# Optimization experiments

Measured on AMD Instinct MI355X. Metric: run time of the kernel, lower is better.

Reference implementation:

```python
import jax, jax.numpy as jnp
import numpy as np

B, T, F, H = 2048, 129, 128, 128  # batch, window, features, hidden


def setup_inputs() -> dict:
    key = jax.random.key(0)
    ks = jax.random.split(key, 7)
    s = 0.05
    return {
        "x": jax.random.normal(ks[0], (B, T - 1, F), jnp.float32),
        "w_lin": jax.random.normal(ks[1], (1, 2 * H + T - 1), jnp.float32) * s,  # attn Linear weight
        "b_lin": jax.random.normal(ks[2], (1,), jnp.float32) * s,
        "w_ih": jax.random.normal(ks[3], (4 * H, F), jnp.float32) * s,  # LSTM input weights (i,f,g,o)
        "w_hh": jax.random.normal(ks[4], (4 * H, H), jnp.float32) * s,
        "b_ih": jax.random.normal(ks[5], (4 * H,), jnp.float32) * s,
        "b_hh": jax.random.normal(ks[6], (4 * H,), jnp.float32) * s,
    }


def _forward(x, w_lin, b_lin, w_ih, w_hh, b_ih, b_hh):
    # x: [B, T-1, F]
    nb, tm1, nf = x.shape
    nh = w_hh.shape[1]
    # Split attention linear weight into the parts applied to h, c, and x-row.
    wh, wc, wx = w_lin[0, :nh], w_lin[0, nh:2 * nh], w_lin[0, 2 * nh:]
    # x.permute(0,2,1) part of the concat is time-invariant: precompute its score.
    s_x = jnp.einsum('btf,t->bf', x, wx)  # [B, F]
    bias = b_ih + b_hh

    def step(carry, xt):
        h, c = carry  # [B, H] each
        # score for feature k = wh.h + wc.c + wx.x[:,k,:] + b  (h/c terms equal for all k)
        scores = (h @ wh + c @ wc + b_lin[0])[:, None] + s_x  # [B, F]
        a = jax.nn.softmax(scores, axis=1)
        xa = a * xt  # attended input at time t, [B, F]
        gates = xa @ w_ih.T + h @ w_hh.T + bias  # [B, 4H]
        i, f, g, o = jnp.split(gates, 4, axis=1)  # torch LSTM gate order
        c_new = jax.nn.sigmoid(f) * c + jax.nn.sigmoid(i) * jnp.tanh(g)
        h_new = jax.nn.sigmoid(o) * jnp.tanh(c_new)
        return (h_new, c_new), (xa, h_new)

    h0 = jnp.zeros((nb, nh), x.dtype)
    _, (xa_seq, h_seq) = jax.lax.scan(step, (h0, h0), x.transpose(1, 0, 2))
    x_atn = xa_seq.transpose(1, 0, 2)  # [B, T-1, F]
    x_enc = h_seq.transpose(1, 0, 2)   # [B, T-1, H]
    return x_atn, x_enc


def reference(x, w_lin, b_lin, w_ih, w_hh, b_ih, b_hh):
    return _forward(x, w_lin, b_lin, w_ih, w_hh, b_ih, b_hh)
```

## Files before the change

### kernel.cpp

```cpp
#include <hip/hip_runtime.h>
#include <hip/hip_bf16.h>

typedef __attribute__((ext_vector_type(8))) short bf16x8;
typedef __attribute__((ext_vector_type(4))) float f32x4;

#define NB 2048
#define TT 128
#define FF 128
#define HH 128
#define NG 512

__device__ __forceinline__ unsigned short f2bf(float x) {
  union { float f; unsigned u; } v; v.f = x;
  unsigned r = (v.u + 0x7fffu + ((v.u >> 16) & 1u)) >> 16;
  return (unsigned short)r;
}
__device__ __forceinline__ unsigned cvtpk_bf16(float lo, float hi) {
  unsigned r;
  asm("v_cvt_pk_bf16_f32 %0, %1, %2" : "=v"(r) : "v"(lo), "v"(hi));
  return r;
}
__device__ __forceinline__ float frcp(float x) { return __builtin_amdgcn_rcpf(x); }
__device__ __forceinline__ float sigf(float x) { return frcp(1.f + __expf(-x)); }
__device__ __forceinline__ float tanh_(float x) {
  float e = __expf(-2.f * x);
  return (1.f - e) * frcp(1.f + e);
}
__device__ __forceinline__ unsigned swzb(int row, int kbyte) {
  return (unsigned)(row * 256 + (kbyte ^ ((row & 7) << 4)));
}
__device__ __forceinline__ void barrier_lds() {
  asm volatile("s_waitcnt lgkmcnt(0)\n\ts_barrier" ::: "memory");
}

__global__ void k_prep(const float* __restrict__ w_ih, const float* __restrict__ w_hh,
                       const float* __restrict__ b_ih, const float* __restrict__ b_hh,
                       unsigned short* __restrict__ wihb, unsigned short* __restrict__ whhb,
                       float* __restrict__ bias) {
  int g = blockIdx.x * blockDim.x + threadIdx.x;
  int gs = gridDim.x * blockDim.x;
  for (int i = g; i < NG * FF; i += gs) {
    wihb[i] = f2bf(w_ih[i]);
    whhb[i] = f2bf(w_hh[i]);
  }
  if (g < NG) bias[g] = b_ih[g] + b_hh[g];
}

__global__ __launch_bounds__(512, 1) void k_rnn_fused(const unsigned short* __restrict__ whhb,
                                                      const unsigned short* __restrict__ wihb,
                                                      const float* __restrict__ bias,
                                                      const float* __restrict__ x,
                                                      const float* __restrict__ w_lin,
                                                      float* __restrict__ xaout_base,
                                                      float* __restrict__ enc) {
  __shared__ unsigned char hLds[2][2048];
  __shared__ unsigned char xLds[2][2048];
  __shared__ float wxs[TT];
  __shared__ float aRow[8][FF];
  int tid = threadIdx.x;
  int l = tid & 63, w = tid >> 6;
  int lg = l >> 4;
  bool low = (lg < 2);
  int b0 = blockIdx.x * 8;
  int kl = w * 16 + (l & 15);
  int ar = l & 7;

  if (tid < TT) wxs[tid] = w_lin[2 * HH + tid];
  ((unsigned*)hLds)[tid] = 0u;
  ((unsigned*)hLds)[tid + 512] = 0u;
  __syncthreads();

  {
    int f4 = l & 31, tpar = l >> 5;
    const float4* xb4 = (const float4*)(x + (size_t)(b0 + w) * TT * FF);
    float4 acc[8];
#pragma unroll
    for (int u = 0; u < 8; ++u) acc[u] = (float4){0.f, 0.f, 0.f, 0.f};
#pragma unroll
    for (int j = 0; j < 64; j += 8) {
      float4 v[8];
#pragma unroll
      for (int u = 0; u < 8; ++u) v[u] = xb4[(tpar + 2 * (j + u)) * 32 + f4];
#pragma unroll
      for (int u = 0; u < 8; ++u) {
        float wt = wxs[tpar + 2 * (j + u)];
        acc[u].x += v[u].x * wt; acc[u].y += v[u].y * wt;
        acc[u].z += v[u].z * wt; acc[u].w += v[u].w * wt;
      }
    }
#pragma unroll
    for (int u = 4; u < 8; ++u) {
      acc[u - 4].x += acc[u].x; acc[u - 4].y += acc[u].y;
      acc[u - 4].z += acc[u].z; acc[u - 4].w += acc[u].w;
    }
    float sx = acc[0].x + acc[1].x + acc[2].x + acc[3].x;
    float sy = acc[0].y + acc[1].y + acc[2].y + acc[3].y;
    float sz = acc[0].z + acc[1].z + acc[2].z + acc[3].z;
    float sw = acc[0].w + acc[1].w + acc[2].w + acc[3].w;
    sx += __shfl_xor(sx, 32); sy += __shfl_xor(sy, 32);
    sz += __shfl_xor(sz, 32); sw += __shfl_xor(sw, 32);
    float m = fmaxf(fmaxf(sx, sy), fmaxf(sz, sw));
#pragma unroll
    for (int d = 1; d < 32; d <<= 1) m = fmaxf(m, __shfl_xor(m, d));
    float e0 = __expf(sx - m), e1 = __expf(sy - m);
    float e2 = __expf(sz - m), e3 = __expf(sw - m);
    float sum = e0 + e1 + e2 + e3;
#pragma unroll
    for (int d = 1; d < 32; d <<= 1) sum += __shfl_xor(sum, d);
    float inv = frcp(sum);
    float4 av; av.x = e0 * inv; av.y = e1 * inv; av.z = e2 * inv; av.w = e3 * inv;
    if (l < 32) *(float4*)(&aRow[w][f4 * 4]) = av;
  }
  barrier_lds();

  bf16x8 Bf[4][8];
  f32x4 bv0, bv1, bv2, bv3;
  {
    float bc0 = bias[0 * 128 + kl], bc1 = bias[1 * 128 + kl];
    float bc2 = bias[2 * 128 + kl], bc3 = bias[3 * 128 + kl];
    bv0 = (f32x4){bc0, bc0, bc0, bc0};
    bv1 = (f32x4){bc1, bc1, bc1, bc1};
    bv2 = (f32x4){bc2, bc2, bc2, bc2};
    bv3 = (f32x4){bc3, bc3, bc3, bc3};
  }
#pragma unroll
  for (int g = 0; g < 4; ++g) {
    int n = g * 128 + kl;
#pragma unroll
    for (int ks = 0; ks < 4; ++ks) {
      Bf[g][ks]     = *(const bf16x8*)(whhb + (size_t)n * HH + ks * 32 + lg * 8);
      Bf[g][4 + ks] = *(const bf16x8*)(wihb + (size_t)n * FF + ks * 32 + lg * 8);
    }
  }

  int srow = tid >> 6, sf = (tid & 63) * 2;
  const float* xrow = x + (size_t)(b0 + srow) * TT * FF + sf;
  float* xaout = xaout_base + (size_t)(b0 + srow) * TT * FF + sf;
  float a0 = aRow[srow][sf], a1 = aRow[srow][sf + 1];

  float2 v0p = *(const float2*)(xrow);
  float2 v1p = *(const float2*)(xrow + FF);
  float2 pv  = *(const float2*)(xrow + 2 * FF);
  float xa00 = v0p.x * a0, xa01 = v0p.y * a1;
  float xa10 = v1p.x * a0, xa11 = v1p.y * a1;
  *(float2*)(xaout)      = (float2){xa00, xa01};
  *(float2*)(xaout + FF) = (float2){xa10, xa11};
  *(unsigned*)(xLds[0] + swzb(srow, sf * 2)) = cvtpk_bf16(xa00, xa01);
  *(unsigned*)(xLds[1] + swzb(srow, sf * 2)) = cvtpk_bf16(xa10, xa11);
  barrier_lds();

  f32x4 xaccA0, xaccA1, xaccA2, xaccA3;
  f32x4 xaccB0, xaccB1, xaccB2, xaccB3;
  {
    bf16x8 Ax[4];
#pragma unroll
    for (int ks = 0; ks < 4; ++ks)
      Ax[ks] = *(const bf16x8*)(xLds[0] + swzb(ar, ks * 64 + lg * 16));
    xaccA0 = bv0; xaccA1 = bv1; xaccA2 = bv2; xaccA3 = bv3;
#pragma unroll
    for (int ks = 0; ks < 4; ++ks) {
      xaccA0 = __builtin_amdgcn_mfma_f32_16x16x32_bf16(Ax[ks], Bf[0][4 + ks], xaccA0, 0, 0, 0);
      xaccA1 = __builtin_amdgcn_mfma_f32_16x16x32_bf16(Ax[ks], Bf[1][4 + ks], xaccA1, 0, 0, 0);
      xaccA2 = __builtin_amdgcn_mfma_f32_16x16x32_bf16(Ax[ks], Bf[2][4 + ks], xaccA2, 0, 0, 0);
      xaccA3 = __builtin_amdgcn_mfma_f32_16x16x32_bf16(Ax[ks], Bf[3][4 + ks], xaccA3, 0, 0, 0);
    }
  }
  barrier_lds();

  int bq0 = ((lg & 1) << 2) | ((lg >> 1) << 1);
  float c0 = 0.f, c1 = 0.f;
  float* pA = enc + (size_t)(b0 + bq0) * TT * HH + kl;
  float* pB = enc + (size_t)(b0 + bq0 + 1) * TT * HH + kl;

#define RNN_BODY(tc, CUR, NXT, XU0, XU1, XU2, XU3, XN0, XN1, XN2, XN3)          \
  {                                                                              \
        \
    float xv0 = pv.x * a0, xv1 = pv.y * a1;                                      \
    *(unsigned*)(xLds[CUR] + swzb(srow, sf * 2)) = cvtpk_bf16(xv0, xv1);         \
    if ((tc) + 2 < TT) *(float2*)(xaout + (size_t)((tc) + 2) * FF) = (float2){xv0, xv1}; \
    int tnx = ((tc) + 3 < TT) ? (tc) + 3 : TT - 1;                               \
    pv = *(const float2*)(xrow + (size_t)tnx * FF);                              \
    bf16x8 Ah[4], Ax[4];                                                         \
    _Pragma("unroll")                                                            \
    for (int ks = 0; ks < 4; ++ks)                                               \
      Ah[ks] = *(const bf16x8*)(hLds[CUR] + swzb(ar, ks * 64 + lg * 16));        \
    _Pragma("unroll")                                                            \
    for (int ks = 0; ks < 4; ++ks)                                               \
      Ax[ks] = *(const bf16x8*)(xLds[NXT] + swzb(ar, ks * 64 + lg * 16));        \
            \
    f32x4 s0_ = XU0, s1_ = XU1, s2_ = XU2, s3_ = XU3;                            \
    _Pragma("unroll")                                                            \
    for (int ks = 0; ks < 4; ++ks) {                                             \
      s0_ = __builtin_amdgcn_mfma_f32_16x16x32_bf16(Ah[ks], Bf[0][ks], s0_, 0,0,0);\
      s1_ = __builtin_amdgcn_mfma_f32_16x16x32_bf16(Ah[ks], Bf[1][ks], s1_, 0,0,0);\
      s2_ = __builtin_amdgcn_mfma_f32_16x16x32_bf16(Ah[ks], Bf[2][ks], s2_, 0,0,0);\
      s3_ = __builtin_amdgcn_mfma_f32_16x16x32_bf16(Ah[ks], Bf[3][ks], s3_, 0,0,0);\
    }                                                                            \
         \
    XN0 = bv0; XN1 = bv1; XN2 = bv2; XN3 = bv3;                                  \
    _Pragma("unroll")                                                            \
    for (int ks = 0; ks < 4; ++ks) {                                             \
      XN0 = __builtin_amdgcn_mfma_f32_16x16x32_bf16(Ax[ks], Bf[0][4+ks], XN0, 0,0,0);\
      XN1 = __builtin_amdgcn_mfma_f32_16x16x32_bf16(Ax[ks], Bf[1][4+ks], XN1, 0,0,0);\
      XN2 = __builtin_amdgcn_mfma_f32_16x16x32_bf16(Ax[ks], Bf[2][4+ks], XN2, 0,0,0);\
      XN3 = __builtin_amdgcn_mfma_f32_16x16x32_bf16(Ax[ks], Bf[3][4+ks], XN3, 0,0,0);\
    }                                                                            \
    float giA = low ? s0_[0] : s0_[2], giB = low ? s0_[1] : s0_[3];              \
    float gfA = low ? s1_[0] : s1_[2], gfB = low ? s1_[1] : s1_[3];              \
    float ggA = low ? s2_[0] : s2_[2], ggB = low ? s2_[1] : s2_[3];              \
    float goA = low ? s3_[0] : s3_[2], goB = low ? s3_[1] : s3_[3];              \
    float cnA = sigf(gfA) * c0 + sigf(giA) * tanh_(ggA);                         \
    float cnB = sigf(gfB) * c1 + sigf(giB) * tanh_(ggB);                         \
    c0 = cnA; c1 = cnB;                                                          \
    float hvA = sigf(goA) * tanh_(cnA);                                          \
    float hvB = sigf(goB) * tanh_(cnB);                                          \
    unsigned hp = cvtpk_bf16(hvA, hvB);                                          \
    unsigned hq = hp >> 16;                                                      \
    *(unsigned short*)(hLds[NXT] + swzb(bq0, kl * 2)) = (unsigned short)hp;      \
    *(unsigned short*)(hLds[NXT] + swzb(bq0 + 1, kl * 2)) = (unsigned short)hq;  \
    pA[(size_t)(tc) * HH] = hvA;                                                 \
    pB[(size_t)(tc) * HH] = hvB;                                                 \
    barrier_lds();                                                               \
  }

  for (int t = 0; t < TT; t += 2) {
    RNN_BODY(t,     0, 1, xaccA0, xaccA1, xaccA2, xaccA3, xaccB0, xaccB1, xaccB2, xaccB3)
    RNN_BODY(t + 1, 1, 0, xaccB0, xaccB1, xaccB2, xaccB3, xaccA0, xaccA1, xaccA2, xaccA3)
  }
#undef RNN_BODY
}

extern "C" void kernel_launch(void* const* d_in, const int* in_sizes, int n_in,
                              void* d_out, int out_size, void* d_ws, size_t ws_size,
                              hipStream_t stream) {
  (void)in_sizes; (void)n_in; (void)out_size; (void)ws_size;
  const float* x     = (const float*)d_in[0];
  const float* w_lin = (const float*)d_in[1];
  const float* w_ih  = (const float*)d_in[3];
  const float* w_hh  = (const float*)d_in[4];
  const float* b_ih  = (const float*)d_in[5];
  const float* b_hh  = (const float*)d_in[6];
  float* out = (float*)d_out;

  char* ws = (char*)d_ws;
  float* bias          = (float*)ws;
  unsigned short* wihb = (unsigned short*)(ws + 4096);
  unsigned short* whhb = (unsigned short*)(ws + 4096 + (1 << 17));

  float* enc = out + (size_t)NB * TT * FF;

  k_prep<<<dim3(64), dim3(256), 0, stream>>>(w_ih, w_hh, b_ih, b_hh, wihb, whhb, bias);
  k_rnn_fused<<<dim3(256), dim3(512), 0, stream>>>(whhb, wihb, bias, x, w_lin, out, enc);
}
```

Baseline: 156.9 us.

## Split LSTM block into recurrent and input-projection warp groups via LDS handoff

Doubles the block to 1024 threads, with 8 waves computing the recurrent h·W_hh gates and the LSTM cell, and 8 other waves computing the attended-input projection xa·W_ih for the next step. The input projection is passed through an LDS buffer, and single-buffered h/x LDS uses two barriers per step. Each wave now holds only half the weight fragments, which cuts register pressure and lets the input GEMM run on separate waves. In exchange it adds a second barrier per timestep and an LDS round trip for the gate pre-activations on the serial critical path.

```diff
diff --git a/kernel.cpp b/kernel.cpp
--- a/kernel.cpp
+++ b/kernel.cpp
@@ -9,6 +9,7 @@
 #define FF 128
 #define HH 128
 #define NG 512
+#define XST 20
 
 __device__ __forceinline__ unsigned short f2bf(float x) {
   union { float f; unsigned u; } v; v.f = x;
@@ -46,33 +47,36 @@
   if (g < NG) bias[g] = b_ih[g] + b_hh[g];
 }
 
-__global__ __launch_bounds__(512, 1) void k_rnn_fused(const unsigned short* __restrict__ whhb,
-                                                      const unsigned short* __restrict__ wihb,
-                                                      const float* __restrict__ bias,
-                                                      const float* __restrict__ x,
-                                                      const float* __restrict__ w_lin,
-                                                      float* __restrict__ xaout_base,
-                                                      float* __restrict__ enc) {
-  __shared__ unsigned char hLds[2][2048];
-  __shared__ unsigned char xLds[2][2048];
+__global__ __launch_bounds__(1024, 4) void k_rnn_fused(const unsigned short* __restrict__ whhb,
+                                                       const unsigned short* __restrict__ wihb,
+                                                       const float* __restrict__ bias,
+                                                       const float* __restrict__ x,
+                                                       const float* __restrict__ w_lin,
+                                                       float* __restrict__ xaout_base,
+                                                       float* __restrict__ enc) {
+  __shared__ unsigned char hLds[2048];
+  __shared__ unsigned char xLds[2048];
   __shared__ float wxs[TT];
   __shared__ float aRow[8][FF];
+  __shared__ float xacc[8 * 64 * XST];
+
   int tid = threadIdx.x;
-  int l = tid & 63, w = tid >> 6;
+  int l = tid & 63, wv = tid >> 6;
+  bool isx = (wv >= 8);
+  int wq = wv & 7;
   int lg = l >> 4;
   bool low = (lg < 2);
   int b0 = blockIdx.x * 8;
-  int kl = w * 16 + (l & 15);
+  int kl = wq * 16 + (l & 15);
   int ar = l & 7;
 
   if (tid < TT) wxs[tid] = w_lin[2 * HH + tid];
-  ((unsigned*)hLds)[tid] = 0u;
-  ((unsigned*)hLds)[tid + 512] = 0u;
+  if (tid < 512) ((unsigned*)hLds)[tid] = 0u;
   __syncthreads();
 
-  {
+  if (!isx) {
     int f4 = l & 31, tpar = l >> 5;
-    const float4* xb4 = (const float4*)(x + (size_t)(b0 + w) * TT * FF);
+    const float4* xb4 = (const float4*)(x + (size_t)(b0 + wq) * TT * FF);
     float4 acc[8];
 #pragma unroll
     for (int u = 0; u < 8; ++u) acc[u] = (float4){0.f, 0.f, 0.f, 0.f};
@@ -109,125 +113,137 @@
     for (int d = 1; d < 32; d <<= 1) sum += __shfl_xor(sum, d);
     float inv = frcp(sum);
     float4 av; av.x = e0 * inv; av.y = e1 * inv; av.z = e2 * inv; av.w = e3 * inv;
-    if (l < 32) *(float4*)(&aRow[w][f4 * 4]) = av;
+    if (l < 32) *(float4*)(&aRow[wq][f4 * 4]) = av;
   }
   barrier_lds();
 
-  bf16x8 Bf[4][8];
+  bf16x8 Wt[4][4];
+  {
+    const unsigned short* wsrc = isx ? wihb : whhb;
+#pragma unroll
+    for (int g = 0; g < 4; ++g) {
+      int n = g * 128 + kl;
+#pragma unroll
+      for (int ks = 0; ks < 4; ++ks)
+        Wt[g][ks] = *(const bf16x8*)(wsrc + (size_t)n * HH + ks * 32 + lg * 8);
+    }
+  }
   f32x4 bv0, bv1, bv2, bv3;
   {
-    float bc0 = bias[0 * 128 + kl], bc1 = bias[1 * 128 + kl];
-    float bc2 = bias[2 * 128 + kl], bc3 = bias[3 * 128 + kl];
+    float bc0 = bias[kl], bc1 = bias[128 + kl];
+    float bc2 = bias[256 + kl], bc3 = bias[384 + kl];
     bv0 = (f32x4){bc0, bc0, bc0, bc0};
     bv1 = (f32x4){bc1, bc1, bc1, bc1};
     bv2 = (f32x4){bc2, bc2, bc2, bc2};
     bv3 = (f32x4){bc3, bc3, bc3, bc3};
   }
-#pragma unroll
-  for (int g = 0; g < 4; ++g) {
-    int n = g * 128 + kl;
-#pragma unroll
-    for (int ks = 0; ks < 4; ++ks) {
-      Bf[g][ks]     = *(const bf16x8*)(whhb + (size_t)n * HH + ks * 32 + lg * 8);
-      Bf[g][4 + ks] = *(const bf16x8*)(wihb + (size_t)n * FF + ks * 32 + lg * 8);
-    }
-  }
-
-  int srow = tid >> 6, sf = (tid & 63) * 2;
-  const float* xrow = x + (size_t)(b0 + srow) * TT * FF + sf;
-  float* xaout = xaout_base + (size_t)(b0 + srow) * TT * FF + sf;
-  float a0 = aRow[srow][sf], a1 = aRow[srow][sf + 1];
-
-  float2 v0p = *(const float2*)(xrow);
-  float2 v1p = *(const float2*)(xrow + FF);
-  float2 pv  = *(const float2*)(xrow + 2 * FF);
-  float xa00 = v0p.x * a0, xa01 = v0p.y * a1;
-  float xa10 = v1p.x * a0, xa11 = v1p.y * a1;
-  *(float2*)(xaout)      = (float2){xa00, xa01};
-  *(float2*)(xaout + FF) = (float2){xa10, xa11};
-  *(unsigned*)(xLds[0] + swzb(srow, sf * 2)) = cvtpk_bf16(xa00, xa01);
-  *(unsigned*)(xLds[1] + swzb(srow, sf * 2)) = cvtpk_bf16(xa10, xa11);
+
+  int sf = l * 2;
+  const float* xrow = x + (size_t)(b0 + wq) * TT * FF + sf;
+  float* xaout = xaout_base + (size_t)(b0 + wq) * TT * FF + sf;
+  float a0 = 0.f, a1 = 0.f;
+  float2 pv = (float2){0.f, 0.f};
+  float* xaccp = &xacc[(wq * 64 + l) * XST];
+
+  if (isx) {
+    a0 = aRow[wq][sf]; a1 = aRow[wq][sf + 1];
+    float2 v0p = *(const float2*)(xrow);
+    float xa00 = v0p.x * a0, xa01 = v0p.y * a1;
+    *(float2*)(xaout) = (float2){xa00, xa01};
+    *(unsigned*)(xLds + swzb(wq, sf * 2)) = cvtpk_bf16(xa00, xa01);
+    pv = *(const float2*)(xrow + FF);
+  }
   barrier_lds();
 
-  f32x4 xaccA0, xaccA1, xaccA2, xaccA3;
-  f32x4 xaccB0, xaccB1, xaccB2, xaccB3;
   {
-    bf16x8 Ax[4];
-#pragma unroll
-    for (int ks = 0; ks < 4; ++ks)
-      Ax[ks] = *(const bf16x8*)(xLds[0] + swzb(ar, ks * 64 + lg * 16));
-    xaccA0 = bv0; xaccA1 = bv1; xaccA2 = bv2; xaccA3 = bv3;
-#pragma unroll
-    for (int ks = 0; ks < 4; ++ks) {
-      xaccA0 = __builtin_amdgcn_mfma_f32_16x16x32_bf16(Ax[ks], Bf[0][4 + ks], xaccA0, 0, 0, 0);
-      xaccA1 = __builtin_amdgcn_mfma_f32_16x16x32_bf16(Ax[ks], Bf[1][4 + ks], xaccA1, 0, 0, 0);
-      xaccA2 = __builtin_amdgcn_mfma_f32_16x16x32_bf16(Ax[ks], Bf[2][4 + ks], xaccA2, 0, 0, 0);
-      xaccA3 = __builtin_amdgcn_mfma_f32_16x16x32_bf16(Ax[ks], Bf[3][4 + ks], xaccA3, 0, 0, 0);
-    }
-  }
-  barrier_lds();
+    bf16x8 AxA[4];
+    if (isx) {
+#pragma unroll
+      for (int ks = 0; ks < 4; ++ks)
+        AxA[ks] = *(const bf16x8*)(xLds + swzb(ar, ks * 64 + lg * 16));
+    }
+    barrier_lds();
+    if (isx) {
+      f32x4 X0 = bv0, X1 = bv1, X2 = bv2, X3 = bv3;
+#pragma unroll
+      for (int ks = 0; ks < 4; ++ks) {
+        X0 = __builtin_amdgcn_mfma_f32_16x16x32_bf16(AxA[ks], Wt[0][ks], X0, 0, 0, 0);
+        X1 = __builtin_amdgcn_mfma_f32_16x16x32_bf16(AxA[ks], Wt[1][ks], X1, 0, 0, 0);
+        X2 = __builtin_amdgcn_mfma_f32_16x16x32_bf16(AxA[ks], Wt[2][ks], X2, 0, 0, 0);
+        X3 = __builtin_amdgcn_mfma_f32_16x16x32_bf16(AxA[ks], Wt[3][ks], X3, 0, 0, 0);
+      }
+      *(f32x4*)(xaccp + 0)  = X0;
+      *(f32x4*)(xaccp + 4)  = X1;
+      *(f32x4*)(xaccp + 8)  = X2;
+      *(f32x4*)(xaccp + 12) = X3;
+      float xa10 = pv.x * a0, xa11 = pv.y * a1;
+      *(float2*)(xaout + FF) = (float2){xa10, xa11};
+      *(unsigned*)(xLds + swzb(wq, sf * 2)) = cvtpk_bf16(xa10, xa11);
+      pv = *(const float2*)(xrow + 2 * FF);
+    }
+    barrier_lds();
+  }
 
   int bq0 = ((lg & 1) << 2) | ((lg >> 1) << 1);
   float c0 = 0.f, c1 = 0.f;
   float* pA = enc + (size_t)(b0 + bq0) * TT * HH + kl;
   float* pB = enc + (size_t)(b0 + bq0 + 1) * TT * HH + kl;
 
-#define RNN_BODY(tc, CUR, NXT, XU0, XU1, XU2, XU3, XN0, XN1, XN2, XN3)          \
-  {                                                                              \
-        \
-    float xv0 = pv.x * a0, xv1 = pv.y * a1;                                      \
-    *(unsigned*)(xLds[CUR] + swzb(srow, sf * 2)) = cvtpk_bf16(xv0, xv1);         \
-    if ((tc) + 2 < TT) *(float2*)(xaout + (size_t)((tc) + 2) * FF) = (float2){xv0, xv1}; \
-    int tnx = ((tc) + 3 < TT) ? (tc) + 3 : TT - 1;                               \
-    pv = *(const float2*)(xrow + (size_t)tnx * FF);                              \
-    bf16x8 Ah[4], Ax[4];                                                         \
-    _Pragma("unroll")                                                            \
-    for (int ks = 0; ks < 4; ++ks)                                               \
-      Ah[ks] = *(const bf16x8*)(hLds[CUR] + swzb(ar, ks * 64 + lg * 16));        \
-    _Pragma("unroll")                                                            \
-    for (int ks = 0; ks < 4; ++ks)                                               \
-      Ax[ks] = *(const bf16x8*)(xLds[NXT] + swzb(ar, ks * 64 + lg * 16));        \
-            \
-    f32x4 s0_ = XU0, s1_ = XU1, s2_ = XU2, s3_ = XU3;                            \
-    _Pragma("unroll")                                                            \
-    for (int ks = 0; ks < 4; ++ks) {                                             \
-      s0_ = __builtin_amdgcn_mfma_f32_16x16x32_bf16(Ah[ks], Bf[0][ks], s0_, 0,0,0);\
-      s1_ = __builtin_amdgcn_mfma_f32_16x16x32_bf16(Ah[ks], Bf[1][ks], s1_, 0,0,0);\
-      s2_ = __builtin_amdgcn_mfma_f32_16x16x32_bf16(Ah[ks], Bf[2][ks], s2_, 0,0,0);\
-      s3_ = __builtin_amdgcn_mfma_f32_16x16x32_bf16(Ah[ks], Bf[3][ks], s3_, 0,0,0);\
-    }                                                                            \
-         \
-    XN0 = bv0; XN1 = bv1; XN2 = bv2; XN3 = bv3;                                  \
-    _Pragma("unroll")                                                            \
-    for (int ks = 0; ks < 4; ++ks) {                                             \
-      XN0 = __builtin_amdgcn_mfma_f32_16x16x32_bf16(Ax[ks], Bf[0][4+ks], XN0, 0,0,0);\
-      XN1 = __builtin_amdgcn_mfma_f32_16x16x32_bf16(Ax[ks], Bf[1][4+ks], XN1, 0,0,0);\
-      XN2 = __builtin_amdgcn_mfma_f32_16x16x32_bf16(Ax[ks], Bf[2][4+ks], XN2, 0,0,0);\
-      XN3 = __builtin_amdgcn_mfma_f32_16x16x32_bf16(Ax[ks], Bf[3][4+ks], XN3, 0,0,0);\
-    }                                                                            \
-    float giA = low ? s0_[0] : s0_[2], giB = low ? s0_[1] : s0_[3];              \
-    float gfA = low ? s1_[0] : s1_[2], gfB = low ? s1_[1] : s1_[3];              \
-    float ggA = low ? s2_[0] : s2_[2], ggB = low ? s2_[1] : s2_[3];              \
-    float goA = low ? s3_[0] : s3_[2], goB = low ? s3_[1] : s3_[3];              \
-    float cnA = sigf(gfA) * c0 + sigf(giA) * tanh_(ggA);                         \
-    float cnB = sigf(gfB) * c1 + sigf(giB) * tanh_(ggB);                         \
-    c0 = cnA; c1 = cnB;                                                          \
-    float hvA = sigf(goA) * tanh_(cnA);                                          \
-    float hvB = sigf(goB) * tanh_(cnB);                                          \
-    unsigned hp = cvtpk_bf16(hvA, hvB);                                          \
-    unsigned hq = hp >> 16;                                                      \
-    *(unsigned short*)(hLds[NXT] + swzb(bq0, kl * 2)) = (unsigned short)hp;      \
-    *(unsigned short*)(hLds[NXT] + swzb(bq0 + 1, kl * 2)) = (unsigned short)hq;  \
-    pA[(size_t)(tc) * HH] = hvA;                                                 \
-    pB[(size_t)(tc) * HH] = hvB;                                                 \
-    barrier_lds();                                                               \
-  }
-
-  for (int t = 0; t < TT; t += 2) {
-    RNN_BODY(t,     0, 1, xaccA0, xaccA1, xaccA2, xaccA3, xaccB0, xaccB1, xaccB2, xaccB3)
-    RNN_BODY(t + 1, 1, 0, xaccB0, xaccB1, xaccB2, xaccB3, xaccA0, xaccA1, xaccA2, xaccA3)
-  }
-#undef RNN_BODY
+  for (int t = 0; t < TT; ++t) {
+    bf16x8 Af[4];
+    f32x4 q0, q1, q2, q3;
+    if (isx) {
+#pragma unroll
+      for (int ks = 0; ks < 4; ++ks)
+        Af[ks] = *(const bf16x8*)(xLds + swzb(ar, ks * 64 + lg * 16));
+      q0 = bv0; q1 = bv1; q2 = bv2; q3 = bv3;
+    } else {
+#pragma unroll
+      for (int ks = 0; ks < 4; ++ks)
+        Af[ks] = *(const bf16x8*)(hLds + swzb(ar, ks * 64 + lg * 16));
+      q0 = *(const f32x4*)(xaccp + 0);
+      q1 = *(const f32x4*)(xaccp + 4);
+      q2 = *(const f32x4*)(xaccp + 8);
+      q3 = *(const f32x4*)(xaccp + 12);
+    }
+    barrier_lds();
+    float xv0 = 0.f, xv1 = 0.f; unsigned spk = 0u;
+    if (isx) { xv0 = pv.x * a0; xv1 = pv.y * a1; spk = cvtpk_bf16(xv0, xv1); }
+#pragma unroll
+    for (int ks = 0; ks < 4; ++ks) {
+      q0 = __builtin_amdgcn_mfma_f32_16x16x32_bf16(Af[ks], Wt[0][ks], q0, 0, 0, 0);
+      q1 = __builtin_amdgcn_mfma_f32_16x16x32_bf16(Af[ks], Wt[1][ks], q1, 0, 0, 0);
+      q2 = __builtin_amdgcn_mfma_f32_16x16x32_bf16(Af[ks], Wt[2][ks], q2, 0, 0, 0);
+      q3 = __builtin_amdgcn_mfma_f32_16x16x32_bf16(Af[ks], Wt[3][ks], q3, 0, 0, 0);
+    }
+    if (isx) {
+      *(f32x4*)(xaccp + 0)  = q0;
+      *(f32x4*)(xaccp + 4)  = q1;
+      *(f32x4*)(xaccp + 8)  = q2;
+      *(f32x4*)(xaccp + 12) = q3;
+      *(unsigned*)(xLds + swzb(wq, sf * 2)) = spk;
+      if (t + 2 < TT) *(float2*)(xaout + (size_t)(t + 2) * FF) = (float2){xv0, xv1};
+      int tnx = (t + 3 < TT) ? t + 3 : TT - 1;
+      pv = *(const float2*)(xrow + (size_t)tnx * FF);
+    } else {
+      float giA = low ? q0[0] : q0[2], giB = low ? q0[1] : q0[3];
+      float gfA = low ? q1[0] : q1[2], gfB = low ? q1[1] : q1[3];
+      float ggA = low ? q2[0] : q2[2], ggB = low ? q2[1] : q2[3];
+      float goA = low ? q3[0] : q3[2], goB = low ? q3[1] : q3[3];
+      float cnA = sigf(gfA) * c0 + sigf(giA) * tanh_(ggA);
+      float cnB = sigf(gfB) * c1 + sigf(giB) * tanh_(ggB);
+      c0 = cnA; c1 = cnB;
+      float hvA = sigf(goA) * tanh_(cnA);
+      float hvB = sigf(goB) * tanh_(cnB);
+      unsigned hp = cvtpk_bf16(hvA, hvB);
+      unsigned hq = hp >> 16;
+      *(unsigned short*)(hLds + swzb(bq0, kl * 2)) = (unsigned short)hp;
+      *(unsigned short*)(hLds + swzb(bq0 + 1, kl * 2)) = (unsigned short)hq;
+      pA[(size_t)t * HH] = hvA;
+      pB[(size_t)t * HH] = hvB;
+    }
+    barrier_lds();
+  }
 }
 
 extern "C" void kernel_launch(void* const* d_in, const int* in_sizes, int n_in,
@@ -250,5 +266,5 @@
   float* enc = out + (size_t)NB * TT * FF;
 
   k_prep<<<dim3(64), dim3(256), 0, stream>>>(w_ih, w_hh, b_ih, b_hh, wihb, whhb, bias);
-  k_rnn_fused<<<dim3(256), dim3(512), 0, stream>>>(whhb, wihb, bias, x, w_lin, out, enc);
-}
+  k_rnn_fused<<<dim3(256), dim3(1024), 0, stream>>>(whhb, wihb, bias, x, w_lin, out, enc);
+}
```

Result: slower. 224.5 us (+43.0%).

## Halve block to 4 waves, each wave handling two 16-column hidden tiles

Applied to the files above, without the earlier changes.

The fused LSTM kernel now runs 256 threads (4 waves) per block instead of 512. Each wave covers 32 hidden columns per gate, holding twice the weight fragments in registers and doing twice the MFMAs per step. The x-score prologue, the xa staging and the gate epilogue are widened so each thread handles two batch rows or a float4. The aim is a cheaper per-step barrier and more independent MFMA chains per wave, at the cost of much higher register pressure and fewer waves to hide latency.

```diff
diff --git a/kernel.cpp b/kernel.cpp
--- a/kernel.cpp
+++ b/kernel.cpp
@@ -46,7 +46,7 @@
   if (g < NG) bias[g] = b_ih[g] + b_hh[g];
 }
 
-__global__ __launch_bounds__(512, 1) void k_rnn_fused(const unsigned short* __restrict__ whhb,
+__global__ __launch_bounds__(256, 1) void k_rnn_fused(const unsigned short* __restrict__ whhb,
                                                       const unsigned short* __restrict__ wihb,
                                                       const float* __restrict__ bias,
                                                       const float* __restrict__ x,
@@ -62,170 +62,219 @@
   int lg = l >> 4;
   bool low = (lg < 2);
   int b0 = blockIdx.x * 8;
-  int kl = w * 16 + (l & 15);
+  int kl0 = w * 32 + (l & 15);
   int ar = l & 7;
 
   if (tid < TT) wxs[tid] = w_lin[2 * HH + tid];
-  ((unsigned*)hLds)[tid] = 0u;
-  ((unsigned*)hLds)[tid + 512] = 0u;
+  ((uint2*)hLds)[tid] = (uint2){0u, 0u};
   __syncthreads();
 
   {
     int f4 = l & 31, tpar = l >> 5;
-    const float4* xb4 = (const float4*)(x + (size_t)(b0 + w) * TT * FF);
-    float4 acc[8];
-#pragma unroll
-    for (int u = 0; u < 8; ++u) acc[u] = (float4){0.f, 0.f, 0.f, 0.f};
+    const float4* xr0 = (const float4*)(x + (size_t)(b0 + 2 * w) * TT * FF);
+    const float4* xr1 = (const float4*)(x + (size_t)(b0 + 2 * w + 1) * TT * FF);
+    float4 ac0[8], ac1[8];
+#pragma unroll
+    for (int u = 0; u < 8; ++u) { ac0[u] = (float4){0,0,0,0}; ac1[u] = (float4){0,0,0,0}; }
 #pragma unroll
     for (int j = 0; j < 64; j += 8) {
-      float4 v[8];
-#pragma unroll
-      for (int u = 0; u < 8; ++u) v[u] = xb4[(tpar + 2 * (j + u)) * 32 + f4];
+      float4 v0[8], v1[8];
+#pragma unroll
+      for (int u = 0; u < 8; ++u) v0[u] = xr0[(tpar + 2 * (j + u)) * 32 + f4];
+#pragma unroll
+      for (int u = 0; u < 8; ++u) v1[u] = xr1[(tpar + 2 * (j + u)) * 32 + f4];
 #pragma unroll
       for (int u = 0; u < 8; ++u) {
         float wt = wxs[tpar + 2 * (j + u)];
-        acc[u].x += v[u].x * wt; acc[u].y += v[u].y * wt;
-        acc[u].z += v[u].z * wt; acc[u].w += v[u].w * wt;
+        ac0[u].x += v0[u].x * wt; ac0[u].y += v0[u].y * wt;
+        ac0[u].z += v0[u].z * wt; ac0[u].w += v0[u].w * wt;
+        ac1[u].x += v1[u].x * wt; ac1[u].y += v1[u].y * wt;
+        ac1[u].z += v1[u].z * wt; ac1[u].w += v1[u].w * wt;
       }
     }
 #pragma unroll
     for (int u = 4; u < 8; ++u) {
-      acc[u - 4].x += acc[u].x; acc[u - 4].y += acc[u].y;
-      acc[u - 4].z += acc[u].z; acc[u - 4].w += acc[u].w;
-    }
-    float sx = acc[0].x + acc[1].x + acc[2].x + acc[3].x;
-    float sy = acc[0].y + acc[1].y + acc[2].y + acc[3].y;
-    float sz = acc[0].z + acc[1].z + acc[2].z + acc[3].z;
-    float sw = acc[0].w + acc[1].w + acc[2].w + acc[3].w;
-    sx += __shfl_xor(sx, 32); sy += __shfl_xor(sy, 32);
-    sz += __shfl_xor(sz, 32); sw += __shfl_xor(sw, 32);
-    float m = fmaxf(fmaxf(sx, sy), fmaxf(sz, sw));
-#pragma unroll
-    for (int d = 1; d < 32; d <<= 1) m = fmaxf(m, __shfl_xor(m, d));
-    float e0 = __expf(sx - m), e1 = __expf(sy - m);
-    float e2 = __expf(sz - m), e3 = __expf(sw - m);
-    float sum = e0 + e1 + e2 + e3;
-#pragma unroll
-    for (int d = 1; d < 32; d <<= 1) sum += __shfl_xor(sum, d);
-    float inv = frcp(sum);
-    float4 av; av.x = e0 * inv; av.y = e1 * inv; av.z = e2 * inv; av.w = e3 * inv;
-    if (l < 32) *(float4*)(&aRow[w][f4 * 4]) = av;
+      ac0[u-4].x += ac0[u].x; ac0[u-4].y += ac0[u].y; ac0[u-4].z += ac0[u].z; ac0[u-4].w += ac0[u].w;
+      ac1[u-4].x += ac1[u].x; ac1[u-4].y += ac1[u].y; ac1[u-4].z += ac1[u].z; ac1[u-4].w += ac1[u].w;
+    }
+    {
+      float sx = ac0[0].x + ac0[1].x + ac0[2].x + ac0[3].x;
+      float sy = ac0[0].y + ac0[1].y + ac0[2].y + ac0[3].y;
+      float sz = ac0[0].z + ac0[1].z + ac0[2].z + ac0[3].z;
+      float sw = ac0[0].w + ac0[1].w + ac0[2].w + ac0[3].w;
+      sx += __shfl_xor(sx, 32); sy += __shfl_xor(sy, 32);
+      sz += __shfl_xor(sz, 32); sw += __shfl_xor(sw, 32);
+      float m = fmaxf(fmaxf(sx, sy), fmaxf(sz, sw));
+#pragma unroll
+      for (int d = 1; d < 32; d <<= 1) m = fmaxf(m, __shfl_xor(m, d));
+      float e0 = __expf(sx - m), e1 = __expf(sy - m);
+      float e2 = __expf(sz - m), e3 = __expf(sw - m);
+      float sum = e0 + e1 + e2 + e3;
+#pragma unroll
+      for (int d = 1; d < 32; d <<= 1) sum += __shfl_xor(sum, d);
+      float inv = frcp(sum);
+      float4 av; av.x = e0 * inv; av.y = e1 * inv; av.z = e2 * inv; av.w = e3 * inv;
+      if (l < 32) *(float4*)(&aRow[2 * w][f4 * 4]) = av;
+    }
+    {
+      float sx = ac1[0].x + ac1[1].x + ac1[2].x + ac1[3].x;
+      float sy = ac1[0].y + ac1[1].y + ac1[2].y + ac1[3].y;
+      float sz = ac1[0].z + ac1[1].z + ac1[2].z + ac1[3].z;
+      float sw = ac1[0].w + ac1[1].w + ac1[2].w + ac1[3].w;
+      sx += __shfl_xor(sx, 32); sy += __shfl_xor(sy, 32);
+      sz += __shfl_xor(sz, 32); sw += __shfl_xor(sw, 32);
+      float m = fmaxf(fmaxf(sx, sy), fmaxf(sz, sw));
+#pragma unroll
+      for (int d = 1; d < 32; d <<= 1) m = fmaxf(m, __shfl_xor(m, d));
+      float e0 = __expf(sx - m), e1 = __expf(sy - m);
+      float e2 = __expf(sz - m), e3 = __expf(sw - m);
+      float sum = e0 + e1 + e2 + e3;
+#pragma unroll
+      for (int d = 1; d < 32; d <<= 1) sum += __shfl_xor(sum, d);
+      float inv = frcp(sum);
+      float4 av; av.x = e0 * inv; av.y = e1 * inv; av.z = e2 * inv; av.w = e3 * inv;
+      if (l < 32) *(float4*)(&aRow[2 * w + 1][f4 * 4]) = av;
+    }
   }
   barrier_lds();
 
-  bf16x8 Bf[4][8];
-  f32x4 bv0, bv1, bv2, bv3;
+  bf16x8 Whh[4][2][4], Wih[4][2][4];
+  float bc[4][2];
+#pragma unroll
+  for (int g = 0; g < 4; ++g)
+#pragma unroll
+    for (int t2 = 0; t2 < 2; ++t2) {
+      int n = g * 128 + kl0 + t2 * 16;
+      bc[g][t2] = bias[n];
+#pragma unroll
+      for (int ks = 0; ks < 4; ++ks) {
+        Whh[g][t2][ks] = *(const bf16x8*)(whhb + (size_t)n * HH + ks * 32 + lg * 8);
+        Wih[g][t2][ks] = *(const bf16x8*)(wihb + (size_t)n * FF + ks * 32 + lg * 8);
+      }
+    }
+
+  int srow = tid >> 5, sf4 = (tid & 31) * 4;
+  const float4* xrow4 = (const float4*)(x + (size_t)(b0 + srow) * TT * FF + sf4);
+  float4* xaout4 = (float4*)(xaout_base + (size_t)(b0 + srow) * TT * FF + sf4);
+  float4 a4 = *(const float4*)(&aRow[srow][sf4]);
+
+  float4 v0p = xrow4[0], v1p = xrow4[32];
+  float4 pv = xrow4[64];
+  float4 xa0, xa1;
+  xa0.x = v0p.x * a4.x; xa0.y = v0p.y * a4.y; xa0.z = v0p.z * a4.z; xa0.w = v0p.w * a4.w;
+  xa1.x = v1p.x * a4.x; xa1.y = v1p.y * a4.y; xa1.z = v1p.z * a4.z; xa1.w = v1p.w * a4.w;
+  xaout4[0] = xa0;
+  xaout4[32] = xa1;
   {
-    float bc0 = bias[0 * 128 + kl], bc1 = bias[1 * 128 + kl];
-    float bc2 = bias[2 * 128 + kl], bc3 = bias[3 * 128 + kl];
-    bv0 = (f32x4){bc0, bc0, bc0, bc0};
-    bv1 = (f32x4){bc1, bc1, bc1, bc1};
-    bv2 = (f32x4){bc2, bc2, bc2, bc2};
-    bv3 = (f32x4){bc3, bc3, bc3, bc3};
-  }
-#pragma unroll
-  for (int g = 0; g < 4; ++g) {
-    int n = g * 128 + kl;
-#pragma unroll
-    for (int ks = 0; ks < 4; ++ks) {
-      Bf[g][ks]     = *(const bf16x8*)(whhb + (size_t)n * HH + ks * 32 + lg * 8);
-      Bf[g][4 + ks] = *(const bf16x8*)(wihb + (size_t)n * FF + ks * 32 + lg * 8);
-    }
-  }
-
-  int srow = tid >> 6, sf = (tid & 63) * 2;
-  const float* xrow = x + (size_t)(b0 + srow) * TT * FF + sf;
-  float* xaout = xaout_base + (size_t)(b0 + srow) * TT * FF + sf;
-  float a0 = aRow[srow][sf], a1 = aRow[srow][sf + 1];
-
-  float2 v0p = *(const float2*)(xrow);
-  float2 v1p = *(const float2*)(xrow + FF);
-  float2 pv  = *(const float2*)(xrow + 2 * FF);
-  float xa00 = v0p.x * a0, xa01 = v0p.y * a1;
-  float xa10 = v1p.x * a0, xa11 = v1p.y * a1;
-  *(float2*)(xaout)      = (float2){xa00, xa01};
-  *(float2*)(xaout + FF) = (float2){xa10, xa11};
-  *(unsigned*)(xLds[0] + swzb(srow, sf * 2)) = cvtpk_bf16(xa00, xa01);
-  *(unsigned*)(xLds[1] + swzb(srow, sf * 2)) = cvtpk_bf16(xa10, xa11);
+    uint2 p0; p0.x = cvtpk_bf16(xa0.x, xa0.y); p0.y = cvtpk_bf16(xa0.z, xa0.w);
+    uint2 p1; p1.x = cvtpk_bf16(xa1.x, xa1.y); p1.y = cvtpk_bf16(xa1.z, xa1.w);
+    *(uint2*)(xLds[0] + swzb(srow, sf4 * 2)) = p0;
+    *(uint2*)(xLds[1] + swzb(srow, sf4 * 2)) = p1;
+  }
   barrier_lds();
 
-  f32x4 xaccA0, xaccA1, xaccA2, xaccA3;
-  f32x4 xaccB0, xaccB1, xaccB2, xaccB3;
+  f32x4 XA[2][4][2];
   {
-    bf16x8 Ax[4];
+    bf16x8 Axf[4];
 #pragma unroll
     for (int ks = 0; ks < 4; ++ks)
-      Ax[ks] = *(const bf16x8*)(xLds[0] + swzb(ar, ks * 64 + lg * 16));
-    xaccA0 = bv0; xaccA1 = bv1; xaccA2 = bv2; xaccA3 = bv3;
-#pragma unroll
-    for (int ks = 0; ks < 4; ++ks) {
-      xaccA0 = __builtin_amdgcn_mfma_f32_16x16x32_bf16(Ax[ks], Bf[0][4 + ks], xaccA0, 0, 0, 0);
-      xaccA1 = __builtin_amdgcn_mfma_f32_16x16x32_bf16(Ax[ks], Bf[1][4 + ks], xaccA1, 0, 0, 0);
-      xaccA2 = __builtin_amdgcn_mfma_f32_16x16x32_bf16(Ax[ks], Bf[2][4 + ks], xaccA2, 0, 0, 0);
-      xaccA3 = __builtin_amdgcn_mfma_f32_16x16x32_bf16(Ax[ks], Bf[3][4 + ks], xaccA3, 0, 0, 0);
-    }
+      Axf[ks] = *(const bf16x8*)(xLds[0] + swzb(ar, ks * 64 + lg * 16));
+#pragma unroll
+    for (int g = 0; g < 4; ++g)
+#pragma unroll
+      for (int t2 = 0; t2 < 2; ++t2)
+        XA[0][g][t2] = (f32x4){bc[g][t2], bc[g][t2], bc[g][t2], bc[g][t2]};
+#pragma unroll
+    for (int ks = 0; ks < 4; ++ks)
+#pragma unroll
+      for (int g = 0; g < 4; ++g)
+#pragma unroll
+        for (int t2 = 0; t2 < 2; ++t2)
+          XA[0][g][t2] = __builtin_amdgcn_mfma_f32_16x16x32_bf16(Axf[ks], Wih[g][t2][ks], XA[0][g][t2], 0, 0, 0);
   }
   barrier_lds();
 
   int bq0 = ((lg & 1) << 2) | ((lg >> 1) << 1);
-  float c0 = 0.f, c1 = 0.f;
-  float* pA = enc + (size_t)(b0 + bq0) * TT * HH + kl;
-  float* pB = enc + (size_t)(b0 + bq0 + 1) * TT * HH + kl;
-
-#define RNN_BODY(tc, CUR, NXT, XU0, XU1, XU2, XU3, XN0, XN1, XN2, XN3)          \
+  float cst[2][2] = {{0.f, 0.f}, {0.f, 0.f}};
+  float* pE[2][2];
+#pragma unroll
+  for (int t2 = 0; t2 < 2; ++t2)
+#pragma unroll
+    for (int r = 0; r < 2; ++r)
+      pE[t2][r] = enc + (size_t)(b0 + bq0 + r) * TT * HH + kl0 + t2 * 16;
+
+#define RNN_BODY(tc, CUR, NXT, PU, PN)                                           \
   {                                                                              \
-        \
-    float xv0 = pv.x * a0, xv1 = pv.y * a1;                                      \
-    *(unsigned*)(xLds[CUR] + swzb(srow, sf * 2)) = cvtpk_bf16(xv0, xv1);         \
-    if ((tc) + 2 < TT) *(float2*)(xaout + (size_t)((tc) + 2) * FF) = (float2){xv0, xv1}; \
+                   \
+    float4 xv;                                                                   \
+    xv.x = pv.x * a4.x; xv.y = pv.y * a4.y;                                      \
+    xv.z = pv.z * a4.z; xv.w = pv.w * a4.w;                                      \
+    uint2 spk; spk.x = cvtpk_bf16(xv.x, xv.y); spk.y = cvtpk_bf16(xv.z, xv.w);   \
+    *(uint2*)(xLds[CUR] + swzb(srow, sf4 * 2)) = spk;                            \
+    if ((tc) + 2 < TT) xaout4[(size_t)((tc) + 2) * 32] = xv;                     \
     int tnx = ((tc) + 3 < TT) ? (tc) + 3 : TT - 1;                               \
-    pv = *(const float2*)(xrow + (size_t)tnx * FF);                              \
-    bf16x8 Ah[4], Ax[4];                                                         \
+    pv = xrow4[(size_t)tnx * 32];                                                \
+    bf16x8 Ah[4], Axf[4];                                                        \
     _Pragma("unroll")                                                            \
     for (int ks = 0; ks < 4; ++ks)                                               \
       Ah[ks] = *(const bf16x8*)(hLds[CUR] + swzb(ar, ks * 64 + lg * 16));        \
     _Pragma("unroll")                                                            \
     for (int ks = 0; ks < 4; ++ks)                                               \
-      Ax[ks] = *(const bf16x8*)(xLds[NXT] + swzb(ar, ks * 64 + lg * 16));        \
-            \
-    f32x4 s0_ = XU0, s1_ = XU1, s2_ = XU2, s3_ = XU3;                            \
-    _Pragma("unroll")                                                            \
-    for (int ks = 0; ks < 4; ++ks) {                                             \
-      s0_ = __builtin_amdgcn_mfma_f32_16x16x32_bf16(Ah[ks], Bf[0][ks], s0_, 0,0,0);\
-      s1_ = __builtin_amdgcn_mfma_f32_16x16x32_bf16(Ah[ks], Bf[1][ks], s1_, 0,0,0);\
-      s2_ = __builtin_amdgcn_mfma_f32_16x16x32_bf16(Ah[ks], Bf[2][ks], s2_, 0,0,0);\
-      s3_ = __builtin_amdgcn_mfma_f32_16x16x32_bf16(Ah[ks], Bf[3][ks], s3_, 0,0,0);\
+      Axf[ks] = *(const bf16x8*)(xLds[NXT] + swzb(ar, ks * 64 + lg * 16));       \
+                  \
+    f32x4 S[4][2];                                                               \
+    _Pragma("unroll")                                                            \
+    for (int g = 0; g < 4; ++g)                                                  \
+      _Pragma("unroll")                                                          \
+      for (int t2 = 0; t2 < 2; ++t2) S[g][t2] = XA[PU][g][t2];                   \
+    _Pragma("unroll")                                                            \
+    for (int ks = 0; ks < 4; ++ks)                                               \
+      _Pragma("unroll")                                                          \
+      for (int g = 0; g < 4; ++g)                                                \
+        _Pragma("unroll")                                                        \
+        for (int t2 = 0; t2 < 2; ++t2)                                           \
+          S[g][t2] = __builtin_amdgcn_mfma_f32_16x16x32_bf16(Ah[ks], Whh[g][t2][ks], S[g][t2], 0, 0, 0); \
+                \
+    _Pragma("unroll")                                                            \
+    for (int g = 0; g < 4; ++g)                                                  \
+      _Pragma("unroll")                                                          \
+      for (int t2 = 0; t2 < 2; ++t2)                                             \
+        XA[PN][g][t2] = (f32x4){bc[g][t2], bc[g][t2], bc[g][t2], bc[g][t2]};     \
+    _Pragma("unroll")                                                            \
+    for (int ks = 0; ks < 4; ++ks)                                               \
+      _Pragma("unroll")                                                          \
+      for (int g = 0; g < 4; ++g)                                                \
+        _Pragma("unroll")                                                        \
+        for (int t2 = 0; t2 < 2; ++t2)                                           \
+          XA[PN][g][t2] = __builtin_amdgcn_mfma_f32_16x16x32_bf16(Axf[ks], Wih[g][t2][ks], XA[PN][g][t2], 0, 0, 0); \
+                                  \
+    _Pragma("unroll")                                                            \
+    for (int t2 = 0; t2 < 2; ++t2) {                                             \
+      float gi0 = low ? S[0][t2][0] : S[0][t2][2];                               \
+      float gi1 = low ? S[0][t2][1] : S[0][t2][3];                               \
+      float gf0 = low ? S[1][t2][0] : S[1][t2][2];                               \
+      float gf1 = low ? S[1][t2][1] : S[1][t2][3];                               \
+      float gg0 = low ? S[2][t2][0] : S[2][t2][2];                               \
+      float gg1 = low ? S[2][t2][1] : S[2][t2][3];                               \
+      float go0 = low ? S[3][t2][0] : S[3][t2][2];                               \
+      float go1 = low ? S[3][t2][1] : S[3][t2][3];                               \
+      float cn0 = sigf(gf0) * cst[t2][0] + sigf(gi0) * tanh_(gg0);               \
+      float cn1 = sigf(gf1) * cst[t2][1] + sigf(gi1) * tanh_(gg1);               \
+      cst[t2][0] = cn0; cst[t2][1] = cn1;                                        \
+      float hv0 = sigf(go0) * tanh_(cn0);                                        \
+      float hv1 = sigf(go1) * tanh_(cn1);                                        \
+      unsigned hp = cvtpk_bf16(hv0, hv1);                                        \
+      *(unsigned short*)(hLds[NXT] + swzb(bq0, (kl0 + t2 * 16) * 2)) = (unsigned short)hp; \
+      *(unsigned short*)(hLds[NXT] + swzb(bq0 + 1, (kl0 + t2 * 16) * 2)) = (unsigned short)(hp >> 16); \
+      pE[t2][0][(size_t)(tc) * HH] = hv0;                                        \
+      pE[t2][1][(size_t)(tc) * HH] = hv1;                                        \
     }                                                                            \
-         \
-    XN0 = bv0; XN1 = bv1; XN2 = bv2; XN3 = bv3;                                  \
-    _Pragma("unroll")                                                            \
-    for (int ks = 0; ks < 4; ++ks) {                                             \
-      XN0 = __builtin_amdgcn_mfma_f32_16x16x32_bf16(Ax[ks], Bf[0][4+ks], XN0, 0,0,0);\
-      XN1 = __builtin_amdgcn_mfma_f32_16x16x32_bf16(Ax[ks], Bf[1][4+ks], XN1, 0,0,0);\
-      XN2 = __builtin_amdgcn_mfma_f32_16x16x32_bf16(Ax[ks], Bf[2][4+ks], XN2, 0,0,0);\
-      XN3 = __builtin_amdgcn_mfma_f32_16x16x32_bf16(Ax[ks], Bf[3][4+ks], XN3, 0,0,0);\
-    }                                                                            \
-    float giA = low ? s0_[0] : s0_[2], giB = low ? s0_[1] : s0_[3];              \
-    float gfA = low ? s1_[0] : s1_[2], gfB = low ? s1_[1] : s1_[3];              \
-    float ggA = low ? s2_[0] : s2_[2], ggB = low ? s2_[1] : s2_[3];              \
-    float goA = low ? s3_[0] : s3_[2], goB = low ? s3_[1] : s3_[3];              \
-    float cnA = sigf(gfA) * c0 + sigf(giA) * tanh_(ggA);                         \
-    float cnB = sigf(gfB) * c1 + sigf(giB) * tanh_(ggB);                         \
-    c0 = cnA; c1 = cnB;                                                          \
-    float hvA = sigf(goA) * tanh_(cnA);                                          \
-    float hvB = sigf(goB) * tanh_(cnB);                                          \
-    unsigned hp = cvtpk_bf16(hvA, hvB);                                          \
-    unsigned hq = hp >> 16;                                                      \
-    *(unsigned short*)(hLds[NXT] + swzb(bq0, kl * 2)) = (unsigned short)hp;      \
-    *(unsigned short*)(hLds[NXT] + swzb(bq0 + 1, kl * 2)) = (unsigned short)hq;  \
-    pA[(size_t)(tc) * HH] = hvA;                                                 \
-    pB[(size_t)(tc) * HH] = hvB;                                                 \
     barrier_lds();                                                               \
   }
 
   for (int t = 0; t < TT; t += 2) {
-    RNN_BODY(t,     0, 1, xaccA0, xaccA1, xaccA2, xaccA3, xaccB0, xaccB1, xaccB2, xaccB3)
-    RNN_BODY(t + 1, 1, 0, xaccB0, xaccB1, xaccB2, xaccB3, xaccA0, xaccA1, xaccA2, xaccA3)
+    RNN_BODY(t,     0, 1, 0, 1)
+    RNN_BODY(t + 1, 1, 0, 1, 0)
   }
 #undef RNN_BODY
 }
@@ -250,5 +299,5 @@
   float* enc = out + (size_t)NB * TT * FF;
 
   k_prep<<<dim3(64), dim3(256), 0, stream>>>(w_ih, w_hh, b_ih, b_hh, wihb, whhb, bias);
-  k_rnn_fused<<<dim3(256), dim3(512), 0, stream>>>(whhb, wihb, bias, x, w_lin, out, enc);
-}
+  k_rnn_fused<<<dim3(256), dim3(256), 0, stream>>>(whhb, wihb, bias, x, w_lin, out, enc);
+}
```

Measured after the change: 241.2 us. +53.7%, slower.
